# Optimization experiments

Hardware: AMD Instinct MI355X
Metric: run time of the kernel (lower is better)

## Reference

```python
import jax, jax.numpy as jnp
import numpy as np

A = 256          # image height (x_shape[0])
B = 256          # image width  (x_shape[1])
N = 64           # filterbank grid size
H_DIM = 1024     # hidden dim
BATCH = 512
MAX_DIM = max(A, B)


def _compute_F(params):
    """Build NxA and NxB Gaussian filterbank matrices from 5 attention params.
    Faithful to the torch code: .item() calls on g_X, g_Y, d cut gradients,
    replicated here with stop_gradient; global (not row-wise) normalization;
    var = exp(params[2] + 1e-8) as in the source."""
    gt_X, gt_Y = params[0], params[1]
    var = jnp.exp(params[2] + 1e-8)
    dt = jnp.exp(params[3])
    g_X = jax.lax.stop_gradient((A + 1) * (gt_X + 1) / 2)
    g_Y = jax.lax.stop_gradient((B + 1) * (gt_Y + 1) / 2)
    d = jax.lax.stop_gradient(dt * (MAX_DIM - 1) / (N - 1))
    sub_val = (-N * 0.5 - 0.5) * d  # first linspace endpoint offset; step == d
    idx = jnp.arange(N, dtype=params.dtype)
    mu_X = g_X + sub_val + d * idx  # == linspace(g_X+sub, g_X+add, N)
    mu_Y = g_Y + sub_val + d * idx
    a = jnp.arange(A, dtype=params.dtype)
    b = jnp.arange(B, dtype=params.dtype)
    F_X = jnp.exp(-(a[None, :] - mu_X[:, None]) ** 2 / (2 * var))  # [N, A]
    F_Y = jnp.exp(-(b[None, :] - mu_Y[:, None]) ** 2 / (2 * var))  # [N, B]
    F_X = F_X / jnp.sum(F_X)
    F_Y = F_Y / jnp.sum(F_Y)
    return F_X, F_Y


def setup_inputs() -> dict:
    key = jax.random.key(0)
    k1, k2, k3, k4, k5 = jax.random.split(key, 5)
    x = jax.random.uniform(k1, (BATCH, A * B), dtype=jnp.float32)
    x_hat = jax.random.normal(k2, (BATCH, A * B), dtype=jnp.float32)
    h = jax.random.normal(k3, (BATCH, H_DIM), dtype=jnp.float32)
    # small init scale keeps exp(params) in a sane range
    W_read_w = jax.random.normal(k4, (5, H_DIM), dtype=jnp.float32) * 0.02
    W_read_b = jax.random.normal(k5, (5,), dtype=jnp.float32) * 0.01
    return {"x": x, "x_hat": x_hat, "h": h, "W_read_w": W_read_w, "W_read_b": W_read_b}


def reference(x, x_hat, h, W_read_w, W_read_b):
    # params from the FIRST batch element only, as in the torch code ([0])
    params = (h @ W_read_w.T + W_read_b)[0]  # [5]
    gamma = jnp.exp(params[4])
    F_X, F_Y = _compute_F(params)
    xi = x.reshape(-1, A, B)
    xh = x_hat.reshape(-1, A, B)

    def filt(im):
        # gamma * F_Y @ im @ F_X^T : [x, N, N]
        return gamma * jnp.einsum('na,xab,mb->xnm', F_Y, im, F_X)

    x_filt = filt(xi).reshape(-1, N * N)
    x_hat_filt = filt(xh).reshape(-1, N * N)
    return jnp.concatenate([x_filt, x_hat_filt], axis=1)  # [batch, 2*N^2]
```

## Files before the change

### kernel.cpp

```cpp
#include <hip/hip_runtime.h>
#include <math.h>

#define N_FILT 64
#define IMG_DIM 256
#define IMG_SZ (256*256)
#define HDIM 1024
#define NBATCH 512


__global__ __launch_bounds__(1024) void k_prep(
    const float* __restrict__ h, const float* __restrict__ Ww,
    const float* __restrict__ Wb, int* __restrict__ meta,
    float* __restrict__ fyg, float* __restrict__ fxg)
{
  __shared__ float red[1024];
  __shared__ float par[8];
  __shared__ float F[N_FILT*IMG_DIM];
  __shared__ int s_lo[64], s_hi[64], s_glo[16], s_ghi[16];
  const int t = threadIdx.x;

  {
    float4 z = make_float4(0.f,0.f,0.f,0.f);
    float4* p1 = (float4*)fyg; float4* p2 = (float4*)fxg;
    #pragma unroll
    for (int k=0;k<4;++k){ p1[t+1024*k]=z; p2[t+1024*k]=z; }
  }

  #pragma unroll
  for (int j=0;j<5;++j){
    red[t] = h[t]*Ww[j*HDIM+t]; __syncthreads();
    for (int o=512;o>0;o>>=1){ if (t<o) red[t]+=red[t+o]; __syncthreads(); }
    if (t==0) par[j]=red[0]+Wb[j];
    __syncthreads();
  }
  const float var   = expf(par[2]+1e-8f);
  const float dt    = expf(par[3]);
  const float gamma = expf(par[4]);
  const float gX = 0.5f*257.f*(par[0]+1.f);
  const float gY = 0.5f*257.f*(par[1]+1.f);
  const float d  = dt*(255.f/63.f);
  const float sub= -32.5f*d;
  const float inv2v = 1.f/(2.f*var);
  const float w88v  = 88.f*var;

  if (t<64){
    float mu = gY + sub + d*(float)t;
    float astar = fminf(255.f, fmaxf(0.f, rintf(mu)));
    float t0 = (astar-mu)*(astar-mu);
    float r  = sqrtf(t0 + w88v);
    int lo = (int)ceilf(mu-r); int hi = (int)floorf(mu+r)+1;
    lo = lo<0?0:lo; hi = hi>256?256:hi; if (hi<lo) hi=lo;
    s_lo[t]=lo; s_hi[t]=hi;
  }
  __syncthreads();
  if (t<16){
    int lo=256, hi=0;
    #pragma unroll
    for (int k2=0;k2<4;++k2){ lo=min(lo,s_lo[t*4+k2]); hi=max(hi,s_hi[t*4+k2]); }
    if (hi<lo){lo=0;hi=0;}
    meta[t]=lo; meta[16+t]=hi; s_glo[t]=lo; s_ghi[t]=hi;
  }
  {
    float sum=0.f;
    #pragma unroll
    for (int k=0;k<16;++k){
      int idx = t + 1024*k;
      int n=idx>>8, a=idx&255;
      float mu = gY + sub + d*(float)n;
      float dx = (float)a - mu;
      float e = expf(-dx*dx*inv2v);
      F[idx]=e; sum+=e;
    }
    red[t]=sum;
  }
  __syncthreads();
  for (int o=512;o>0;o>>=1){ if (t<o) red[t]+=red[t+o]; __syncthreads(); }
  const float scY = gamma/red[0];
  __syncthreads();
  #pragma unroll
  for (int k=0;k<16;++k){
    int idx = t + 1024*k;
    int n=idx>>8, a=idx&255, g=n>>2;
    int lo=s_glo[g], hi=s_ghi[g];
    if (a>=lo && a<hi) fyg[(size_t)((g<<10) + ((a-lo)<<2) + (n&3))] = F[idx]*scY;
  }
  __syncthreads();

  if (t<64){
    float mu = gX + sub + d*(float)t;
    float astar = fminf(255.f, fmaxf(0.f, rintf(mu)));
    float t0 = (astar-mu)*(astar-mu);
    float r  = sqrtf(t0 + w88v);
    int lo = (int)ceilf(mu-r); int hi = (int)floorf(mu+r)+1;
    lo = lo<0?0:lo; hi = hi>256?256:hi; if (hi<lo) hi=lo;
    s_lo[t]=lo; s_hi[t]=hi;
  }
  __syncthreads();
  if (t<16){
    int lo=256, hi=0;
    #pragma unroll
    for (int k2=0;k2<4;++k2){ lo=min(lo,s_lo[t*4+k2]); hi=max(hi,s_hi[t*4+k2]); }
    if (hi<lo){lo=0;hi=0;}
    int lo4 = lo & ~3;
    meta[32+t]=lo4; meta[48+t]=hi; s_glo[t]=lo4; s_ghi[t]=hi;
  }
  {
    float sum2=0.f;
    #pragma unroll
    for (int k=0;k<16;++k){
      int idx = t + 1024*k;
      int m=idx>>8, b=idx&255;
      float mu = gX + sub + d*(float)m;
      float dx=(float)b-mu;
      float e=expf(-dx*dx*inv2v);
      F[idx]=e; sum2+=e;
    }
    red[t]=sum2;
  }
  __syncthreads();
  for (int o=512;o>0;o>>=1){ if (t<o) red[t]+=red[t+o]; __syncthreads(); }
  const float scX = 1.f/red[0];
  __syncthreads();
  #pragma unroll
  for (int k=0;k<16;++k){
    int idx = t + 1024*k;
    int m=idx>>8, b=idx&255, q=m>>2;
    int lo4=s_glo[q], hi=s_ghi[q];
    if (b>=lo4 && b<hi) fxg[(size_t)((q<<10) + ((b-lo4)<<2) + (m&3))] = F[idx]*scX;
  }
}

__global__ __launch_bounds__(256, 8) void k_main(
    const float* __restrict__ x, const float* __restrict__ xh,
    const int* __restrict__ meta, const float* __restrict__ fyg,
    const float* __restrict__ fxg, float* __restrict__ out)
{
  __shared__ float Tt[16*256];
  const int bid = blockIdx.x;
  const int lg  = ((bid&7)<<9) | (bid>>3);
  const int img = lg>>2, qq = lg&3;
  const int tid = threadIdx.x;
  const int w    = __builtin_amdgcn_readfirstlane(tid>>6);
  const int lane = tid & 63;
  const float* __restrict__ src = (img<NBATCH) ? (x  + (size_t)img*IMG_SZ)
                                               : (xh + (size_t)(img-NBATCH)*IMG_SZ);
  float* __restrict__ dst = ((img<NBATCH) ? (out + (size_t)img*8192)
                                          : (out + (size_t)(img-NBATCH)*8192 + 4096))
                            + qq*1024;

  {
    const int g  = qq*4 + w;
    const int a0 = __builtin_amdgcn_readfirstlane(meta[g]);
    const int nr = __builtin_amdgcn_readfirstlane(meta[16+g]) - a0;
    const int C  = (nr + 7) >> 3;
    const float* rp0 = src + 4*lane;
    const float* wp  = fyg + ((size_t)g<<10);
    float acc[4][4];
    #pragma unroll
    for (int k2=0;k2<4;++k2){acc[k2][0]=0.f;acc[k2][1]=0.f;acc[k2][2]=0.f;acc[k2][3]=0.f;}
    for (int c=0; c<C; ++c){
      float4 A[8];
      #pragma unroll
      for (int j=0;j<8;++j){
        int ra = a0 + c*8 + j; ra = ra>255?255:ra;
        A[j] = *(const float4* __restrict__)(rp0 + (ra<<8));
      }
      #pragma unroll
      for (int j=0;j<8;++j){
        int rw = c*8 + j; rw = rw>255?255:rw;
        const float* wr = wp + (rw<<2);
        const float w0=wr[0], w1=wr[1], w2=wr[2], w3=wr[3];
        acc[0][0]=fmaf(w0,A[j].x,acc[0][0]); acc[0][1]=fmaf(w0,A[j].y,acc[0][1]);
        acc[0][2]=fmaf(w0,A[j].z,acc[0][2]); acc[0][3]=fmaf(w0,A[j].w,acc[0][3]);
        acc[1][0]=fmaf(w1,A[j].x,acc[1][0]); acc[1][1]=fmaf(w1,A[j].y,acc[1][1]);
        acc[1][2]=fmaf(w1,A[j].z,acc[1][2]); acc[1][3]=fmaf(w1,A[j].w,acc[1][3]);
        acc[2][0]=fmaf(w2,A[j].x,acc[2][0]); acc[2][1]=fmaf(w2,A[j].y,acc[2][1]);
        acc[2][2]=fmaf(w2,A[j].z,acc[2][2]); acc[2][3]=fmaf(w2,A[j].w,acc[2][3]);
        acc[3][0]=fmaf(w3,A[j].x,acc[3][0]); acc[3][1]=fmaf(w3,A[j].y,acc[3][1]);
        acc[3][2]=fmaf(w3,A[j].z,acc[3][2]); acc[3][3]=fmaf(w3,A[j].w,acc[3][3]);
      }
    }
    #pragma unroll
    for (int k2=0;k2<4;++k2){
      const int n = w*4 + k2;
      float4 v; v.x=acc[k2][0]; v.y=acc[k2][1]; v.z=acc[k2][2]; v.w=acc[k2][3];
      *(float4*)&Tt[(n<<8) + ((lane ^ n)<<2)] = v;
    }
  }
  __syncthreads();

  const int nl = lane & 15;
  const int cc = lane >> 4;
  const int q  = w*4 + cc;
  const int lo4 = meta[32+q];
  const int hi  = meta[48+q];
  const int ng  = (hi - lo4 + 3) >> 2;
  const int u0  = lo4 >> 2;
  const float* wq = fxg + ((size_t)q<<10);
  float o0=0.f,o1=0.f,o2=0.f,o3=0.f;
  #pragma unroll 2
  for (int it=0; it<ng; ++it){
    const int u = u0 + it;
    const float4 tv = *(const float4*)&Tt[(nl<<8) + ((u ^ nl)<<2)];
    const float4 w0 = *(const float4*)(wq + it*16);
    const float4 w1 = *(const float4*)(wq + it*16 + 4);
    const float4 w2 = *(const float4*)(wq + it*16 + 8);
    const float4 w3 = *(const float4*)(wq + it*16 + 12);
    o0=fmaf(tv.x,w0.x,fmaf(tv.y,w1.x,fmaf(tv.z,w2.x,fmaf(tv.w,w3.x,o0))));
    o1=fmaf(tv.x,w0.y,fmaf(tv.y,w1.y,fmaf(tv.z,w2.y,fmaf(tv.w,w3.y,o1))));
    o2=fmaf(tv.x,w0.z,fmaf(tv.y,w1.z,fmaf(tv.z,w2.z,fmaf(tv.w,w3.z,o2))));
    o3=fmaf(tv.x,w0.w,fmaf(tv.y,w1.w,fmaf(tv.z,w2.w,fmaf(tv.w,w3.w,o3))));
  }
  __syncthreads();

  {
    const int m0 = q*4;
    Tt[nl*68 + m0 + 0] = o0; Tt[nl*68 + m0 + 1] = o1;
    Tt[nl*68 + m0 + 2] = o2; Tt[nl*68 + m0 + 3] = o3;
  }
  __syncthreads();
  {
    const int f = tid*4;
    const int n = f>>6, m = f&63;
    const float4 v = *(const float4*)&Tt[n*68+m];
    *(float4*)(dst+f) = v;
  }
}

extern "C" void kernel_launch(void* const* d_in, const int* in_sizes, int n_in,
                              void* d_out, int out_size, void* d_ws, size_t ws_size,
                              hipStream_t stream)
{
  const float* x  = (const float*)d_in[0];
  const float* xh = (const float*)d_in[1];
  const float* h  = (const float*)d_in[2];
  const float* Ww = (const float*)d_in[3];
  const float* Wb = (const float*)d_in[4];
  float* out = (float*)d_out;

  int*   meta = (int*)d_ws;
  float* fyg  = (float*)((char*)d_ws + 256);
  float* fxg  = (float*)((char*)d_ws + 256 + 65536);

  k_prep<<<1, 1024, 0, stream>>>(h, Ww, Wb, meta, fyg, fxg);
  k_main<<<8*NBATCH, 256, 0, stream>>>(x, xh, meta, fyg, fxg, out);
}
```

Measured before the change: 100.3 us.

## Split prep into two blocks and restructure main-kernel load scheduling

The prep kernel now runs as two 256-thread blocks, one per filter side. It uses wave-shuffle reductions instead of 1024-thread shared-memory tree reductions, so the two filterbanks are built in parallel. In the main kernel, the weight loads are hoisted alongside the image loads and separated from the FMAs with sched_barriers. The second-stage loop is unrolled by two with a wave-uniform trip count, and the occupancy hint drops from 8 to 5 waves. The aim is more memory-level parallelism per wave, at the cost of extra registers and lower occupancy.

```diff
diff --git a/kernel.cpp b/kernel.cpp
--- a/kernel.cpp
+++ b/kernel.cpp
@@ -8,43 +8,61 @@
 #define NBATCH 512
 
 
-__global__ __launch_bounds__(1024) void k_prep(
+__global__ __launch_bounds__(256) void k_prep(
     const float* __restrict__ h, const float* __restrict__ Ww,
     const float* __restrict__ Wb, int* __restrict__ meta,
     float* __restrict__ fyg, float* __restrict__ fxg)
 {
-  __shared__ float red[1024];
-  __shared__ float par[8];
+  __shared__ float partial[32];
+  __shared__ float par_s[8];
   __shared__ float F[N_FILT*IMG_DIM];
   __shared__ int s_lo[64], s_hi[64], s_glo[16], s_ghi[16];
-  const int t = threadIdx.x;
+  __shared__ float ssum[4];
+  const int t   = threadIdx.x;
+  const int side= blockIdx.x;
+  const int wv  = t>>6, ln = t&63;
+  float* __restrict__ wout = side ? fxg : fyg;
 
   {
     float4 z = make_float4(0.f,0.f,0.f,0.f);
-    float4* p1 = (float4*)fyg; float4* p2 = (float4*)fxg;
-    #pragma unroll
-    for (int k=0;k<4;++k){ p1[t+1024*k]=z; p2[t+1024*k]=z; }
-  }
-
-  #pragma unroll
-  for (int j=0;j<5;++j){
-    red[t] = h[t]*Ww[j*HDIM+t]; __syncthreads();
-    for (int o=512;o>0;o>>=1){ if (t<o) red[t]+=red[t+o]; __syncthreads(); }
-    if (t==0) par[j]=red[0]+Wb[j];
-    __syncthreads();
-  }
-  const float var   = expf(par[2]+1e-8f);
-  const float dt    = expf(par[3]);
-  const float gamma = expf(par[4]);
-  const float gX = 0.5f*257.f*(par[0]+1.f);
-  const float gY = 0.5f*257.f*(par[1]+1.f);
+    float4* p = (float4*)wout;
+    #pragma unroll
+    for (int k=0;k<16;++k) p[t + 256*k] = z;
+  }
+
+  {
+    float s0=0.f,s1=0.f,s2=0.f,s3=0.f,s4=0.f;
+    for (int k=t;k<HDIM;k+=256){
+      const float hv=h[k];
+      s0=fmaf(hv,Ww[k        ],s0);
+      s1=fmaf(hv,Ww[HDIM+k   ],s1);
+      s2=fmaf(hv,Ww[2*HDIM+k ],s2);
+      s3=fmaf(hv,Ww[3*HDIM+k ],s3);
+      s4=fmaf(hv,Ww[4*HDIM+k ],s4);
+    }
+    #pragma unroll
+    for (int o=32;o>0;o>>=1){
+      s0+=__shfl_down(s0,o); s1+=__shfl_down(s1,o); s2+=__shfl_down(s2,o);
+      s3+=__shfl_down(s3,o); s4+=__shfl_down(s4,o);
+    }
+    if (ln==0){ partial[wv*8+0]=s0; partial[wv*8+1]=s1; partial[wv*8+2]=s2;
+                partial[wv*8+3]=s3; partial[wv*8+4]=s4; }
+  }
+  __syncthreads();
+  if (t<5) par_s[t]=partial[t]+partial[8+t]+partial[16+t]+partial[24+t]+Wb[t];
+  __syncthreads();
+
+  const float var   = expf(par_s[2]+1e-8f);
+  const float dt    = expf(par_s[3]);
+  const float gamma = expf(par_s[4]);
+  const float gC = 0.5f*257.f*(par_s[side?0:1]+1.f);
   const float d  = dt*(255.f/63.f);
   const float sub= -32.5f*d;
   const float inv2v = 1.f/(2.f*var);
   const float w88v  = 88.f*var;
 
   if (t<64){
-    float mu = gY + sub + d*(float)t;
+    float mu = gC + sub + d*(float)t;
     float astar = fminf(255.f, fmaxf(0.f, rintf(mu)));
     float t0 = (astar-mu)*(astar-mu);
     float r  = sqrtf(t0 + w88v);
@@ -58,79 +76,36 @@
     #pragma unroll
     for (int k2=0;k2<4;++k2){ lo=min(lo,s_lo[t*4+k2]); hi=max(hi,s_hi[t*4+k2]); }
     if (hi<lo){lo=0;hi=0;}
-    meta[t]=lo; meta[16+t]=hi; s_glo[t]=lo; s_ghi[t]=hi;
-  }
-  {
-    float sum=0.f;
-    #pragma unroll
-    for (int k=0;k<16;++k){
-      int idx = t + 1024*k;
-      int n=idx>>8, a=idx&255;
-      float mu = gY + sub + d*(float)n;
-      float dx = (float)a - mu;
-      float e = expf(-dx*dx*inv2v);
-      F[idx]=e; sum+=e;
-    }
-    red[t]=sum;
-  }
-  __syncthreads();
-  for (int o=512;o>0;o>>=1){ if (t<o) red[t]+=red[t+o]; __syncthreads(); }
-  const float scY = gamma/red[0];
-  __syncthreads();
+    if (side==0){ meta[t]=lo; meta[16+t]=hi; }
+    else        { lo &= ~3;  meta[32+t]=lo; meta[48+t]=hi; }
+    s_glo[t]=lo; s_ghi[t]=hi;
+  }
+  float sum=0.f;
   #pragma unroll
-  for (int k=0;k<16;++k){
-    int idx = t + 1024*k;
+  for (int k=0;k<64;++k){
+    int idx=t+256*k;
+    int n=idx>>8, a=idx&255;
+    float mu = gC+sub+d*(float)n;
+    float dx=(float)a-mu;
+    float e=expf(-dx*dx*inv2v);
+    F[idx]=e; sum+=e;
+  }
+  #pragma unroll
+  for (int o=32;o>0;o>>=1) sum+=__shfl_down(sum,o);
+  if (ln==0) ssum[wv]=sum;
+  __syncthreads();
+  const float stot = ssum[0]+ssum[1]+ssum[2]+ssum[3];
+  const float sc = (side==0 ? gamma : 1.f)/stot;
+  #pragma unroll
+  for (int k=0;k<64;++k){
+    int idx=t+256*k;
     int n=idx>>8, a=idx&255, g=n>>2;
     int lo=s_glo[g], hi=s_ghi[g];
-    if (a>=lo && a<hi) fyg[(size_t)((g<<10) + ((a-lo)<<2) + (n&3))] = F[idx]*scY;
-  }
-  __syncthreads();
-
-  if (t<64){
-    float mu = gX + sub + d*(float)t;
-    float astar = fminf(255.f, fmaxf(0.f, rintf(mu)));
-    float t0 = (astar-mu)*(astar-mu);
-    float r  = sqrtf(t0 + w88v);
-    int lo = (int)ceilf(mu-r); int hi = (int)floorf(mu+r)+1;
-    lo = lo<0?0:lo; hi = hi>256?256:hi; if (hi<lo) hi=lo;
-    s_lo[t]=lo; s_hi[t]=hi;
-  }
-  __syncthreads();
-  if (t<16){
-    int lo=256, hi=0;
-    #pragma unroll
-    for (int k2=0;k2<4;++k2){ lo=min(lo,s_lo[t*4+k2]); hi=max(hi,s_hi[t*4+k2]); }
-    if (hi<lo){lo=0;hi=0;}
-    int lo4 = lo & ~3;
-    meta[32+t]=lo4; meta[48+t]=hi; s_glo[t]=lo4; s_ghi[t]=hi;
-  }
-  {
-    float sum2=0.f;
-    #pragma unroll
-    for (int k=0;k<16;++k){
-      int idx = t + 1024*k;
-      int m=idx>>8, b=idx&255;
-      float mu = gX + sub + d*(float)m;
-      float dx=(float)b-mu;
-      float e=expf(-dx*dx*inv2v);
-      F[idx]=e; sum2+=e;
-    }
-    red[t]=sum2;
-  }
-  __syncthreads();
-  for (int o=512;o>0;o>>=1){ if (t<o) red[t]+=red[t+o]; __syncthreads(); }
-  const float scX = 1.f/red[0];
-  __syncthreads();
-  #pragma unroll
-  for (int k=0;k<16;++k){
-    int idx = t + 1024*k;
-    int m=idx>>8, b=idx&255, q=m>>2;
-    int lo4=s_glo[q], hi=s_ghi[q];
-    if (b>=lo4 && b<hi) fxg[(size_t)((q<<10) + ((b-lo4)<<2) + (m&3))] = F[idx]*scX;
+    if (a>=lo && a<hi) wout[(size_t)((g<<10)+((a-lo)<<2)+(n&3))] = F[idx]*sc;
   }
 }
 
-__global__ __launch_bounds__(256, 8) void k_main(
+__global__ __launch_bounds__(256, 5) void k_main(
     const float* __restrict__ x, const float* __restrict__ xh,
     const int* __restrict__ meta, const float* __restrict__ fyg,
     const float* __restrict__ fxg, float* __restrict__ out)
@@ -158,27 +133,31 @@
     float acc[4][4];
     #pragma unroll
     for (int k2=0;k2<4;++k2){acc[k2][0]=0.f;acc[k2][1]=0.f;acc[k2][2]=0.f;acc[k2][3]=0.f;}
+    #pragma unroll 1
     for (int c=0; c<C; ++c){
       float4 A[8];
+      float wt0[8], wt1[8], wt2[8], wt3[8];
       #pragma unroll
       for (int j=0;j<8;++j){
         int ra = a0 + c*8 + j; ra = ra>255?255:ra;
         A[j] = *(const float4* __restrict__)(rp0 + (ra<<8));
+        int rw = c*8 + j; rw = rw>255?255:rw;
+        const float* wr = wp + (rw<<2);
+        wt0[j]=wr[0]; wt1[j]=wr[1]; wt2[j]=wr[2]; wt3[j]=wr[3];
       }
+      __builtin_amdgcn_sched_barrier(0);
       #pragma unroll
       for (int j=0;j<8;++j){
-        int rw = c*8 + j; rw = rw>255?255:rw;
-        const float* wr = wp + (rw<<2);
-        const float w0=wr[0], w1=wr[1], w2=wr[2], w3=wr[3];
-        acc[0][0]=fmaf(w0,A[j].x,acc[0][0]); acc[0][1]=fmaf(w0,A[j].y,acc[0][1]);
-        acc[0][2]=fmaf(w0,A[j].z,acc[0][2]); acc[0][3]=fmaf(w0,A[j].w,acc[0][3]);
-        acc[1][0]=fmaf(w1,A[j].x,acc[1][0]); acc[1][1]=fmaf(w1,A[j].y,acc[1][1]);
-        acc[1][2]=fmaf(w1,A[j].z,acc[1][2]); acc[1][3]=fmaf(w1,A[j].w,acc[1][3]);
-        acc[2][0]=fmaf(w2,A[j].x,acc[2][0]); acc[2][1]=fmaf(w2,A[j].y,acc[2][1]);
-        acc[2][2]=fmaf(w2,A[j].z,acc[2][2]); acc[2][3]=fmaf(w2,A[j].w,acc[2][3]);
-        acc[3][0]=fmaf(w3,A[j].x,acc[3][0]); acc[3][1]=fmaf(w3,A[j].y,acc[3][1]);
-        acc[3][2]=fmaf(w3,A[j].z,acc[3][2]); acc[3][3]=fmaf(w3,A[j].w,acc[3][3]);
+        acc[0][0]=fmaf(wt0[j],A[j].x,acc[0][0]); acc[0][1]=fmaf(wt0[j],A[j].y,acc[0][1]);
+        acc[0][2]=fmaf(wt0[j],A[j].z,acc[0][2]); acc[0][3]=fmaf(wt0[j],A[j].w,acc[0][3]);
+        acc[1][0]=fmaf(wt1[j],A[j].x,acc[1][0]); acc[1][1]=fmaf(wt1[j],A[j].y,acc[1][1]);
+        acc[1][2]=fmaf(wt1[j],A[j].z,acc[1][2]); acc[1][3]=fmaf(wt1[j],A[j].w,acc[1][3]);
+        acc[2][0]=fmaf(wt2[j],A[j].x,acc[2][0]); acc[2][1]=fmaf(wt2[j],A[j].y,acc[2][1]);
+        acc[2][2]=fmaf(wt2[j],A[j].z,acc[2][2]); acc[2][3]=fmaf(wt2[j],A[j].w,acc[2][3]);
+        acc[3][0]=fmaf(wt3[j],A[j].x,acc[3][0]); acc[3][1]=fmaf(wt3[j],A[j].y,acc[3][1]);
+        acc[3][2]=fmaf(wt3[j],A[j].z,acc[3][2]); acc[3][3]=fmaf(wt3[j],A[j].w,acc[3][3]);
       }
+      __builtin_amdgcn_sched_barrier(0);
     }
     #pragma unroll
     for (int k2=0;k2<4;++k2){
@@ -194,22 +173,38 @@
   const int q  = w*4 + cc;
   const int lo4 = meta[32+q];
   const int hi  = meta[48+q];
-  const int ng  = (hi - lo4 + 3) >> 2;
+  int ngu = (hi - lo4 + 3) >> 2;
+  ngu = max(ngu, __shfl_xor(ngu,16));
+  ngu = max(ngu, __shfl_xor(ngu,32));
   const int u0  = lo4 >> 2;
   const float* wq = fxg + ((size_t)q<<10);
   float o0=0.f,o1=0.f,o2=0.f,o3=0.f;
-  #pragma unroll 2
-  for (int it=0; it<ng; ++it){
-    const int u = u0 + it;
-    const float4 tv = *(const float4*)&Tt[(nl<<8) + ((u ^ nl)<<2)];
-    const float4 w0 = *(const float4*)(wq + it*16);
-    const float4 w1 = *(const float4*)(wq + it*16 + 4);
-    const float4 w2 = *(const float4*)(wq + it*16 + 8);
-    const float4 w3 = *(const float4*)(wq + it*16 + 12);
-    o0=fmaf(tv.x,w0.x,fmaf(tv.y,w1.x,fmaf(tv.z,w2.x,fmaf(tv.w,w3.x,o0))));
-    o1=fmaf(tv.x,w0.y,fmaf(tv.y,w1.y,fmaf(tv.z,w2.y,fmaf(tv.w,w3.y,o1))));
-    o2=fmaf(tv.x,w0.z,fmaf(tv.y,w1.z,fmaf(tv.z,w2.z,fmaf(tv.w,w3.z,o2))));
-    o3=fmaf(tv.x,w0.w,fmaf(tv.y,w1.w,fmaf(tv.z,w2.w,fmaf(tv.w,w3.w,o3))));
+  #pragma unroll 1
+  for (int it=0; it<ngu; it+=2){
+    const int uA = min(u0+it,   63);
+    const int uB = min(u0+it+1, 63);
+    const float4 tvA = *(const float4*)&Tt[(nl<<8) + ((uA ^ nl)<<2)];
+    const float4 tvB = *(const float4*)&Tt[(nl<<8) + ((uB ^ nl)<<2)];
+    const float4 a0w = *(const float4*)(wq + it*16);
+    const float4 a1w = *(const float4*)(wq + it*16 + 4);
+    const float4 a2w = *(const float4*)(wq + it*16 + 8);
+    const float4 a3w = *(const float4*)(wq + it*16 + 12);
+    const float4 b0w = *(const float4*)(wq + it*16 + 16);
+    const float4 b1w = *(const float4*)(wq + it*16 + 20);
+    const float4 b2w = *(const float4*)(wq + it*16 + 24);
+    const float4 b3w = *(const float4*)(wq + it*16 + 28);
+    __builtin_amdgcn_sched_barrier(0);
+    o0=fmaf(tvA.x,a0w.x,fmaf(tvA.y,a1w.x,fmaf(tvA.z,a2w.x,fmaf(tvA.w,a3w.x,o0))));
+    o1=fmaf(tvA.x,a0w.y,fmaf(tvA.y,a1w.y,fmaf(tvA.z,a2w.y,fmaf(tvA.w,a3w.y,o1))));
+    o2=fmaf(tvA.x,a0w.z,fmaf(tvA.y,a1w.z,fmaf(tvA.z,a2w.z,fmaf(tvA.w,a3w.z,o2))));
+    o3=fmaf(tvA.x,a0w.w,fmaf(tvA.y,a1w.w,fmaf(tvA.z,a2w.w,fmaf(tvA.w,a3w.w,o3))));
+    if (it+1 < ngu){
+      o0=fmaf(tvB.x,b0w.x,fmaf(tvB.y,b1w.x,fmaf(tvB.z,b2w.x,fmaf(tvB.w,b3w.x,o0))));
+      o1=fmaf(tvB.x,b0w.y,fmaf(tvB.y,b1w.y,fmaf(tvB.z,b2w.y,fmaf(tvB.w,b3w.y,o1))));
+      o2=fmaf(tvB.x,b0w.z,fmaf(tvB.y,b1w.z,fmaf(tvB.z,b2w.z,fmaf(tvB.w,b3w.z,o2))));
+      o3=fmaf(tvB.x,b0w.w,fmaf(tvB.y,b1w.w,fmaf(tvB.z,b2w.w,fmaf(tvB.w,b3w.w,o3))));
+    }
+    __builtin_amdgcn_sched_barrier(0);
   }
   __syncthreads();
 
@@ -242,6 +237,6 @@
   float* fyg  = (float*)((char*)d_ws + 256);
   float* fxg  = (float*)((char*)d_ws + 256 + 65536);
 
-  k_prep<<<1, 1024, 0, stream>>>(h, Ww, Wb, meta, fyg, fxg);
+  k_prep<<<2, 256, 0, stream>>>(h, Ww, Wb, meta, fyg, fxg);
   k_main<<<8*NBATCH, 256, 0, stream>>>(x, xh, meta, fyg, fxg, out);
 }
```

New measurement: 96.63 us. -3.6%, faster.
